# Kernel tuning notes

Measured on AMD Instinct MI355X. Metric: run time of the kernel, lower is better.

The kernel has to match this reference:

```python
import jax, jax.numpy as jnp
import numpy as np

EPS = 1e-05

def setup_inputs() -> dict:
    key = jax.random.key(0)
    k1, k2 = jax.random.split(key)
    B, C, H, W = 4, 512, 128, 128
    content_feat = jax.random.normal(k1, (B, C, H, W), dtype=jnp.float32)
    style_feat = jax.random.normal(k2, (B, C, H, W), dtype=jnp.float32)
    return {"content_feat": content_feat, "style_feat": style_feat}

def _cov(flat_centered, n):
    # flat_centered: [B, C, N] -> [B, C, C]
    C = flat_centered.shape[1]
    cov = jnp.einsum('bcn,bdn->bcd', flat_centered, flat_centered) / (n - 1)
    return cov + EPS * jnp.eye(C, dtype=flat_centered.dtype)

def reference(content_feat, style_feat):
    B, C, H, W = content_feat.shape
    N = H * W

    # --- whitening (content) ---
    cf = content_feat.reshape(B, C, -1)
    c_mean = jnp.mean(cf, axis=2, keepdims=True)
    c_cent = cf - c_mean
    c_cov = _cov(c_cent, N)
    u, s, vh = jnp.linalg.svd(c_cov)  # torch.svd's v == vh.T
    # u @ diag(s^-0.5) @ v^T @ c_cent
    whitened = jnp.einsum('bij,bj,bjk,bkn->bin', u, s ** -0.5, vh, c_cent)

    # --- coloring (style) ---
    sf = style_feat.reshape(B, C, -1)
    s_mean = jnp.mean(sf, axis=2, keepdims=True)
    s_cent = sf - s_mean
    s_cov = _cov(s_cent, N)
    su, ss, svh = jnp.linalg.svd(s_cov)
    colored = jnp.einsum('bij,bj,bjk,bkn->bin', su, jnp.sqrt(ss), svh, whitened)
    colored = colored + s_mean
    return colored.reshape(style_feat.shape)
```

## Files before the change

kernel.cpp:

```cpp
#include <hip/hip_runtime.h>


typedef unsigned short u16;
typedef __attribute__((ext_vector_type(8))) short bf16x8;
typedef __attribute__((ext_vector_type(4))) float f32x4;

__device__ __forceinline__ u16 f2bf(float f) {
  unsigned u = __float_as_uint(f);
  u += 0x7fffu + ((u >> 16) & 1u);
  return (u16)(u >> 16);
}

__device__ __forceinline__ void async_cp16(const u16* g, u16* l) {
  __builtin_amdgcn_global_load_lds((__attribute__((address_space(1))) void*)g,
                                   (__attribute__((address_space(3))) void*)l,
                                   16, 0, 0);
}

template<int BM, int BN, int FM, int FN>
__device__ __forceinline__ void gemm_nt(const u16* __restrict__ A, int lda,
                                        const u16* __restrict__ B, int ldb,
                                        int K, f32x4 (&acc)[FM][FN],
                                        u16* lA, u16* lB) {
  const int t = threadIdx.x;
  const int lane = t & 63;
  const int wid = t >> 6;
  const int wm = wid & 1, wn = wid >> 1;
  const int l16 = lane & 15, quad = lane >> 4;
  f32x4 zero = {0.f, 0.f, 0.f, 0.f};
#pragma unroll
  for (int im = 0; im < FM; ++im)
#pragma unroll
    for (int in = 0; in < FN; ++in) acc[im][in] = zero;

  constexpr int CA = (BM * 64) / (256 * 8);
  constexpr int CB = (BN * 64) / (256 * 8);

  for (int k0 = 0; k0 < K; k0 += 64) {
#pragma unroll
    for (int i = 0; i < CA; ++i) {
      int chunk = t + i * 256;
      async_cp16(A + (size_t)(chunk >> 3) * lda + k0 + (chunk & 7) * 8, lA + chunk * 8);
    }
#pragma unroll
    for (int i = 0; i < CB; ++i) {
      int chunk = t + i * 256;
      async_cp16(B + (size_t)(chunk >> 3) * ldb + k0 + (chunk & 7) * 8, lB + chunk * 8);
    }
    __syncthreads();
#pragma unroll
    for (int ks = 0; ks < 2; ++ks) {
      bf16x8 af[FM], bfr[FN];
#pragma unroll
      for (int im = 0; im < FM; ++im)
        af[im] = *(const bf16x8*)(lA + (wm * FM * 16 + im * 16 + l16) * 64 + ks * 32 + quad * 8);
#pragma unroll
      for (int in = 0; in < FN; ++in)
        bfr[in] = *(const bf16x8*)(lB + (wn * FN * 16 + in * 16 + l16) * 64 + ks * 32 + quad * 8);
#pragma unroll
      for (int im = 0; im < FM; ++im)
#pragma unroll
        for (int in = 0; in < FN; ++in)
          acc[im][in] = __builtin_amdgcn_mfma_f32_16x16x32_bf16(af[im], bfr[in], acc[im][in], 0, 0, 0);
    }
    __syncthreads();
  }
}

__global__ __launch_bounds__(256) void k_means_convert(
    const float* __restrict__ xc, const float* __restrict__ xs,
    u16* __restrict__ xcb, u16* __restrict__ xsb, float* __restrict__ mu) {
  int bx = blockIdx.x;
  int feat = bx >> 11;
  int row = bx & 2047;
  const float* src = (feat ? xs : xc) + (size_t)row * 16384;
  u16* dst = (feat ? xsb : xcb) + (size_t)row * 16384;
  int t = threadIdx.x;
  float s = 0.f;
#pragma unroll
  for (int i = 0; i < 16; ++i) {
    int idx = (t + i * 256) * 4;
    float4 v = *(const float4*)(src + idx);
    s += (v.x + v.y) + (v.z + v.w);
    ushort4 o;
    o.x = f2bf(v.x); o.y = f2bf(v.y); o.z = f2bf(v.z); o.w = f2bf(v.w);
    *(ushort4*)(dst + idx) = o;
  }
  __shared__ float red[256];
  red[t] = s;
  __syncthreads();
  for (int off = 128; off > 0; off >>= 1) {
    if (t < off) red[t] += red[t + off];
    __syncthreads();
  }
  if (t == 0) mu[bx] = red[0] * (1.f / 16384.f);
}

__global__ __launch_bounds__(256) void k_gram(
    const u16* __restrict__ xcb, const u16* __restrict__ xsb,
    const float* __restrict__ mu, float* __restrict__ cov) {
  __shared__ u16 lA[128 * 64], lB[128 * 64];
  const int tile = blockIdx.x, split = blockIdx.y, mat = blockIdx.z;
  const int tm = tile & 3, tn = tile >> 2;
  const u16* X = (mat >= 4 ? xsb : xcb) + (size_t)(mat & 3) * 512 * 16384;
  const u16* A = X + (size_t)tm * 128 * 16384 + split * 2048;
  const u16* B = X + (size_t)tn * 128 * 16384 + split * 2048;
  f32x4 acc[4][4];
  gemm_nt<128, 128, 4, 4>(A, 16384, B, 16384, 2048, acc, lA, lB);
  const int lane = threadIdx.x & 63, wid = threadIdx.x >> 6;
  const int wm = wid & 1, wn = wid >> 1, l16 = lane & 15, quad = lane >> 4;
  const float* muf = mu + (mat >> 2) * 2048 + (mat & 3) * 512;
  float* C = cov + (size_t)mat * 262144;
  const float scale = 1.f / 16383.f;
  const bool base = (split == 0);
#pragma unroll
  for (int im = 0; im < 4; ++im)
#pragma unroll
    for (int in = 0; in < 4; ++in)
#pragma unroll
      for (int i = 0; i < 4; ++i) {
        int gm = tm * 128 + wm * 64 + im * 16 + quad * 4 + i;
        int gn = tn * 128 + wn * 64 + in * 16 + l16;
        float v = acc[im][in][i] * scale;
        if (base) v += (gm == gn ? 1e-5f : 0.f) - (16384.f / 16383.f) * muf[gm] * muf[gn];
        atomicAdd(C + gm * 512 + gn, v);
      }
}

__global__ __launch_bounds__(256) void k_bound(const float* __restrict__ cov,
                                               float* __restrict__ lam) {
  const int mat = blockIdx.x, t = threadIdx.x;
  const float* A = cov + (size_t)mat * 262144;
  float mx = 0.f;
  for (int rr = 0; rr < 2; ++rr) {
    const float4* row = (const float4*)(A + (size_t)(t + rr * 256) * 512);
    float s = 0.f;
#pragma unroll 8
    for (int j = 0; j < 128; ++j) {
      float4 v = row[j];
      s += fabsf(v.x) + fabsf(v.y) + fabsf(v.z) + fabsf(v.w);
    }
    mx = fmaxf(mx, s);
  }
  __shared__ float red[256];
  red[t] = mx;
  __syncthreads();
  for (int off = 128; off > 0; off >>= 1) {
    if (t < off) red[t] = fmaxf(red[t], red[t + off]);
    __syncthreads();
  }
  if (t == 0) lam[mat] = red[0];
}

__global__ __launch_bounds__(256) void k_nsinit(
    const float* __restrict__ cov, const float* __restrict__ lam,
    const float* __restrict__ mu, float* __restrict__ Yfp, float* __restrict__ Zfp,
    u16* __restrict__ Ybf, u16* __restrict__ Zbf, float* __restrict__ bias) {
  int bx = blockIdx.x;
  if (bx >= 8192) {
    int i = (bx - 8192) * 256 + threadIdx.x;
    bias[i] = mu[2048 + i];
    return;
  }
  int mat = bx >> 10;
  int idx = (bx & 1023) * 256 + threadIdx.x;
  int i = idx >> 9, j = idx & 511;
  size_t g = (size_t)mat * 262144 + idx;
  float a = cov[g] / lam[mat];
  float z = (i == j) ? 1.f : 0.f;
  Yfp[g] = a; Zfp[g] = z;
  Ybf[g] = f2bf(a); Zbf[g] = f2bf(z);
}

__global__ __launch_bounds__(256) void k_ns1(const u16* __restrict__ Zbf,
                                             const u16* __restrict__ Ybf,
                                             u16* __restrict__ Dbf) {
  __shared__ u16 lA[64 * 64], lB[64 * 64];
  const int tile = blockIdx.x, mat = blockIdx.z;
  const int tm = tile & 7, tn = tile >> 3;
  const u16* A = Zbf + (size_t)mat * 262144 + tm * 64 * 512;
  const u16* B = Ybf + (size_t)mat * 262144 + tn * 64 * 512;
  f32x4 acc[2][2];
  gemm_nt<64, 64, 2, 2>(A, 512, B, 512, 512, acc, lA, lB);
  const int lane = threadIdx.x & 63, wid = threadIdx.x >> 6;
  const int wm = wid & 1, wn = wid >> 1, l16 = lane & 15, quad = lane >> 4;
  u16* D = Dbf + (size_t)mat * 262144;
#pragma unroll
  for (int im = 0; im < 2; ++im)
#pragma unroll
    for (int in = 0; in < 2; ++in)
#pragma unroll
      for (int i = 0; i < 4; ++i) {
        int gm = tm * 64 + wm * 32 + im * 16 + quad * 4 + i;
        int gn = tn * 64 + wn * 32 + in * 16 + l16;
        float d = 0.5f * ((gm == gn ? 1.f : 0.f) - acc[im][in][i]);
        D[gm * 512 + gn] = f2bf(d);
      }
}

__global__ __launch_bounds__(256) void k_ns2(
    const u16* __restrict__ Ybf, const u16* __restrict__ Zbf, const u16* __restrict__ Dbf,
    float* __restrict__ Yfp, float* __restrict__ Zfp,
    u16* __restrict__ Ybn, u16* __restrict__ Zbn) {
  __shared__ u16 lA[64 * 64], lB[64 * 64];
  const int tile = blockIdx.x, z = blockIdx.z;
  const int kind = z >> 3, mat = z & 7;
  const int tm = tile & 7, tn = tile >> 3;
  size_t mo = (size_t)mat * 262144;
  const u16* A; const u16* B; float* M; u16* O;
  if (kind == 0) { A = Ybf + mo; B = Dbf + mo; M = Yfp + mo; O = Ybn + mo; }
  else           { A = Dbf + mo; B = Zbf + mo; M = Zfp + mo; O = Zbn + mo; }
  f32x4 acc[2][2];
  gemm_nt<64, 64, 2, 2>(A + tm * 64 * 512, 512, B + tn * 64 * 512, 512, 512, acc, lA, lB);
  const int lane = threadIdx.x & 63, wid = threadIdx.x >> 6;
  const int wm = wid & 1, wn = wid >> 1, l16 = lane & 15, quad = lane >> 4;
#pragma unroll
  for (int im = 0; im < 2; ++im)
#pragma unroll
    for (int in = 0; in < 2; ++in)
#pragma unroll
      for (int i = 0; i < 4; ++i) {
        int gm = tm * 64 + wm * 32 + im * 16 + quad * 4 + i;
        int gn = tn * 64 + wn * 32 + in * 16 + l16;
        float v = acc[im][in][i] + M[gm * 512 + gn];
        M[gm * 512 + gn] = v;
        O[gm * 512 + gn] = f2bf(v);
      }
}

__global__ __launch_bounds__(256) void k_transpose(const u16* __restrict__ Xcb,
                                                   u16* __restrict__ Xct) {
  __shared__ u16 tb[64][72];
  const int t = threadIdx.x;
  const size_t base = (size_t)blockIdx.z * 512 * 16384;
  const int n0 = blockIdx.x * 64, c0 = blockIdx.y * 64;
#pragma unroll
  for (int i = 0; i < 2; ++i) {
    int chunk = t + i * 256;
    int r = chunk >> 3, cc = chunk & 7;
    uint4 v = *(const uint4*)(Xcb + base + (size_t)(c0 + r) * 16384 + n0 + cc * 8);
    const u16* e = (const u16*)&v;
#pragma unroll
    for (int j = 0; j < 8; ++j) tb[cc * 8 + j][r] = e[j];
  }
  __syncthreads();
  const size_t obase = (size_t)blockIdx.z * 16384 * 512;
#pragma unroll
  for (int i = 0; i < 2; ++i) {
    int chunk = t + i * 256;
    int r = chunk >> 3, cc = chunk & 7;
    u16 tmp[8];
#pragma unroll
    for (int j = 0; j < 8; ++j) tmp[j] = tb[r][cc * 8 + j];
    *(uint4*)(Xct + obase + (size_t)(n0 + r) * 512 + c0 + cc * 8) = *(const uint4*)tmp;
  }
}

__global__ __launch_bounds__(256) void k_compose(
    const u16* __restrict__ Ybf, const u16* __restrict__ Zbf,
    const float* __restrict__ lam, const float* __restrict__ mu,
    float* __restrict__ bias, u16* __restrict__ Tbf) {
  __shared__ u16 lA[128 * 64], lB[128 * 64];
  const int tile = blockIdx.x, b = blockIdx.z;
  const int tm = tile & 3, tn = tile >> 2;
  const u16* A = Ybf + (size_t)(4 + b) * 262144 + tm * 128 * 512;
  const u16* B = Zbf + (size_t)b * 262144 + tn * 128 * 512;
  f32x4 acc[4][4];
  gemm_nt<128, 128, 4, 4>(A, 512, B, 512, 512, acc, lA, lB);
  const int lane = threadIdx.x & 63, wid = threadIdx.x >> 6;
  const int wm = wid & 1, wn = wid >> 1, l16 = lane & 15, quad = lane >> 4;
  const float scale = sqrtf(lam[4 + b] / lam[b]);
  const float* muc = mu + b * 512;
  u16* T = Tbf + (size_t)b * 262144;
#pragma unroll
  for (int im = 0; im < 4; ++im)
#pragma unroll
    for (int i = 0; i < 4; ++i) {
      int gm = tm * 128 + wm * 64 + im * 16 + quad * 4 + i;
      float s = 0.f;
#pragma unroll
      for (int in = 0; in < 4; ++in) {
        int gn = tn * 128 + wn * 64 + in * 16 + l16;
        float tv = acc[im][in][i] * scale;
        T[gm * 512 + gn] = f2bf(tv);
        s += tv * muc[gn];
      }
      atomicAdd(&bias[b * 512 + gm], -s);
    }
}

__global__ __launch_bounds__(256) void k_apply(
    const u16* __restrict__ Tbf, const u16* __restrict__ Xct,
    const float* __restrict__ bias, float* __restrict__ out) {
  __shared__ u16 lA[128 * 64], lB[128 * 64];
  const int bx = blockIdx.x, b = blockIdx.z;
  const int tm = bx & 3, tn = bx >> 2;
  const u16* A = Tbf + (size_t)b * 262144 + tm * 128 * 512;
  const u16* B = Xct + (size_t)b * 16384 * 512 + (size_t)tn * 128 * 512;
  f32x4 acc[4][4];
  gemm_nt<128, 128, 4, 4>(A, 512, B, 512, 512, acc, lA, lB);
  const int lane = threadIdx.x & 63, wid = threadIdx.x >> 6;
  const int wm = wid & 1, wn = wid >> 1, l16 = lane & 15, quad = lane >> 4;
#pragma unroll
  for (int im = 0; im < 4; ++im)
#pragma unroll
    for (int in = 0; in < 4; ++in)
#pragma unroll
      for (int i = 0; i < 4; ++i) {
        int gm = tm * 128 + wm * 64 + im * 16 + quad * 4 + i;
        int gn = tn * 128 + wn * 64 + in * 16 + l16;
        out[((size_t)b * 512 + gm) * 16384 + gn] = acc[im][in][i] + bias[b * 512 + gm];
      }
}

extern "C" void kernel_launch(void* const* d_in, const int* in_sizes, int n_in,
                              void* d_out, int out_size, void* d_ws, size_t ws_size,
                              hipStream_t stream) {
  (void)in_sizes; (void)n_in; (void)out_size; (void)ws_size;
  const float* xc = (const float*)d_in[0];
  const float* xs = (const float*)d_in[1];
  float* out = (float*)d_out;
  char* w = (char*)d_ws;

  u16*   XA   = (u16*)(w);
  u16*   XB   = (u16*)(w + 67108864);
  float* cov  = (float*)(w + 134217728);
  float* Yfp  = (float*)(w + 142606336);
  float* Zfp  = (float*)(w + 150994944);
  u16*   Ybf0 = (u16*)(w + 159383552);
  u16*   Ybf1 = (u16*)(w + 163577856);
  u16*   Zbf0 = (u16*)(w + 167772160);
  u16*   Zbf1 = (u16*)(w + 171966464);
  u16*   Dbf  = (u16*)(w + 176160768);
  u16*   Tbf  = (u16*)(w + 180355072);
  float* mu   = (float*)(w + 182452224);
  float* lam  = (float*)(w + 182468608);
  float* bias = (float*)(w + 182468864);

  hipMemsetAsync(cov, 0, 8388608, stream);
  k_means_convert<<<4096, 256, 0, stream>>>(xc, xs, XA, XB, mu);
  k_gram<<<dim3(16, 8, 8), 256, 0, stream>>>(XA, XB, mu, cov);
  k_bound<<<8, 256, 0, stream>>>(cov, lam);
  k_nsinit<<<8200, 256, 0, stream>>>(cov, lam, mu, Yfp, Zfp, Ybf0, Zbf0, bias);
  k_transpose<<<dim3(256, 8, 4), 256, 0, stream>>>(XA, XB);

  u16 *Yc = Ybf0, *Yn = Ybf1, *Zc = Zbf0, *Zn = Zbf1;
  for (int it = 0; it < 8; ++it) {
    k_ns1<<<dim3(64, 1, 8), 256, 0, stream>>>(Zc, Yc, Dbf);
    k_ns2<<<dim3(64, 1, 16), 256, 0, stream>>>(Yc, Zc, Dbf, Yfp, Zfp, Yn, Zn);
    u16* t1 = Yc; Yc = Yn; Yn = t1;
    u16* t2 = Zc; Zc = Zn; Zn = t2;
  }

  k_compose<<<dim3(16, 1, 4), 256, 0, stream>>>(Yc, Zc, lam, mu, bias, Tbf);
  k_apply<<<dim3(512, 1, 4), 256, 0, stream>>>(Tbf, XB, bias, out);
}
```

Baseline: 923.7 us.

## Swizzle LDS layout, enlarge gram tiles with diagonal reuse, cut one NS iteration

The shared GEMM core now XOR-swizzles LDS rows to avoid bank conflicts, and its tile size, thread count and warp grid are templated. The Gram kernel moves to 256x256 tiles with 512 threads, and diagonal tiles reuse the A tile instead of staging B. The Newton-Schulz loop drops from 8 to 7 iterations, which removes work but may reduce the accuracy of the inverse square root. Larger tiles reduce the number of blocks and raise register pressure in the Gram kernel.

After: 871.7 us. -5.6%, faster.

```diff
diff --git a/kernel.cpp b/kernel.cpp
--- a/kernel.cpp
+++ b/kernel.cpp
@@ -17,35 +17,42 @@
                                    16, 0, 0);
 }
 
-template<int BM, int BN, int FM, int FN>
-__device__ __forceinline__ void gemm_nt(const u16* __restrict__ A, int lda,
-                                        const u16* __restrict__ B, int ldb,
-                                        int K, f32x4 (&acc)[FM][FN],
-                                        u16* lA, u16* lB) {
+template<int BM, int BN, int FM, int FN, int NT, int WM, int WN>
+__device__ __forceinline__ void gemm_core(const u16* __restrict__ A, int lda,
+                                          const u16* __restrict__ B, int ldb,
+                                          int K, f32x4 (&acc)[FM][FN],
+                                          u16* lA, u16* lB, bool stageB) {
   const int t = threadIdx.x;
   const int lane = t & 63;
   const int wid = t >> 6;
-  const int wm = wid & 1, wn = wid >> 1;
+  const int wm = wid % WM, wn = wid / WM;
   const int l16 = lane & 15, quad = lane >> 4;
+  const int sw = l16 & 7;
   f32x4 zero = {0.f, 0.f, 0.f, 0.f};
 #pragma unroll
   for (int im = 0; im < FM; ++im)
 #pragma unroll
     for (int in = 0; in < FN; ++in) acc[im][in] = zero;
 
-  constexpr int CA = (BM * 64) / (256 * 8);
-  constexpr int CB = (BN * 64) / (256 * 8);
+  constexpr int CA = (BM * 8) / NT;
+  constexpr int CB = (BN * 8) / NT;
 
   for (int k0 = 0; k0 < K; k0 += 64) {
 #pragma unroll
     for (int i = 0; i < CA; ++i) {
-      int chunk = t + i * 256;
-      async_cp16(A + (size_t)(chunk >> 3) * lda + k0 + (chunk & 7) * 8, lA + chunk * 8);
-    }
-#pragma unroll
-    for (int i = 0; i < CB; ++i) {
-      int chunk = t + i * 256;
-      async_cp16(B + (size_t)(chunk >> 3) * ldb + k0 + (chunk & 7) * 8, lB + chunk * 8);
+      int c = t + i * NT;
+      int row = c >> 3;
+      int src = (c & 7) ^ (row & 7);
+      async_cp16(A + (size_t)row * lda + k0 + src * 8, lA + c * 8);
+    }
+    if (stageB) {
+#pragma unroll
+      for (int i = 0; i < CB; ++i) {
+        int c = t + i * NT;
+        int row = c >> 3;
+        int src = (c & 7) ^ (row & 7);
+        async_cp16(B + (size_t)row * ldb + k0 + src * 8, lB + c * 8);
+      }
     }
     __syncthreads();
 #pragma unroll
@@ -53,10 +60,12 @@
       bf16x8 af[FM], bfr[FN];
 #pragma unroll
       for (int im = 0; im < FM; ++im)
-        af[im] = *(const bf16x8*)(lA + (wm * FM * 16 + im * 16 + l16) * 64 + ks * 32 + quad * 8);
+        af[im] = *(const bf16x8*)(lA + ((wm * FM + im) * 16 + l16) * 64 +
+                                  (((ks * 4 + quad) ^ sw) * 8));
 #pragma unroll
       for (int in = 0; in < FN; ++in)
-        bfr[in] = *(const bf16x8*)(lB + (wn * FN * 16 + in * 16 + l16) * 64 + ks * 32 + quad * 8);
+        bfr[in] = *(const bf16x8*)(lB + ((wn * FN + in) * 16 + l16) * 64 +
+                                   (((ks * 4 + quad) ^ sw) * 8));
 #pragma unroll
       for (int im = 0; im < FM; ++im)
 #pragma unroll
@@ -96,31 +105,33 @@
   if (t == 0) mu[bx] = red[0] * (1.f / 16384.f);
 }
 
-__global__ __launch_bounds__(256) void k_gram(
+__global__ __launch_bounds__(512, 2) void k_gram(
     const u16* __restrict__ xcb, const u16* __restrict__ xsb,
     const float* __restrict__ mu, float* __restrict__ cov) {
-  __shared__ u16 lA[128 * 64], lB[128 * 64];
+  __shared__ u16 lds[2 * 256 * 64];
   const int tile = blockIdx.x, split = blockIdx.y, mat = blockIdx.z;
-  const int tm = tile & 3, tn = tile >> 2;
+  const int tm = tile & 1, tn = tile >> 1;
   const u16* X = (mat >= 4 ? xsb : xcb) + (size_t)(mat & 3) * 512 * 16384;
-  const u16* A = X + (size_t)tm * 128 * 16384 + split * 2048;
-  const u16* B = X + (size_t)tn * 128 * 16384 + split * 2048;
-  f32x4 acc[4][4];
-  gemm_nt<128, 128, 4, 4>(A, 16384, B, 16384, 2048, acc, lA, lB);
-  const int lane = threadIdx.x & 63, wid = threadIdx.x >> 6;
-  const int wm = wid & 1, wn = wid >> 1, l16 = lane & 15, quad = lane >> 4;
+  const u16* A = X + (size_t)tm * 256 * 16384 + split * 2048;
+  const u16* B = X + (size_t)tn * 256 * 16384 + split * 2048;
+  u16* lA = lds;
+  u16* lB = (tm == tn) ? lds : lds + 256 * 64;
+  f32x4 acc[8][4];
+  gemm_core<256, 256, 8, 4, 512, 2, 4>(A, 16384, B, 16384, 2048, acc, lA, lB, tm != tn);
+  const int lane = threadIdx.x & 63, wid = threadIdx.x >> 6;
+  const int wm = wid % 2, wn = wid / 2, l16 = lane & 15, quad = lane >> 4;
   const float* muf = mu + (mat >> 2) * 2048 + (mat & 3) * 512;
   float* C = cov + (size_t)mat * 262144;
   const float scale = 1.f / 16383.f;
   const bool base = (split == 0);
 #pragma unroll
-  for (int im = 0; im < 4; ++im)
+  for (int im = 0; im < 8; ++im)
 #pragma unroll
     for (int in = 0; in < 4; ++in)
 #pragma unroll
       for (int i = 0; i < 4; ++i) {
-        int gm = tm * 128 + wm * 64 + im * 16 + quad * 4 + i;
-        int gn = tn * 128 + wn * 64 + in * 16 + l16;
+        int gm = tm * 256 + wm * 128 + im * 16 + quad * 4 + i;
+        int gn = tn * 256 + wn * 64 + in * 16 + l16;
         float v = acc[im][in][i] * scale;
         if (base) v += (gm == gn ? 1e-5f : 0.f) - (16384.f / 16383.f) * muf[gm] * muf[gn];
         atomicAdd(C + gm * 512 + gn, v);
@@ -175,15 +186,15 @@
 __global__ __launch_bounds__(256) void k_ns1(const u16* __restrict__ Zbf,
                                              const u16* __restrict__ Ybf,
                                              u16* __restrict__ Dbf) {
-  __shared__ u16 lA[64 * 64], lB[64 * 64];
+  __shared__ u16 lds[2 * 64 * 64];
   const int tile = blockIdx.x, mat = blockIdx.z;
   const int tm = tile & 7, tn = tile >> 3;
   const u16* A = Zbf + (size_t)mat * 262144 + tm * 64 * 512;
   const u16* B = Ybf + (size_t)mat * 262144 + tn * 64 * 512;
   f32x4 acc[2][2];
-  gemm_nt<64, 64, 2, 2>(A, 512, B, 512, 512, acc, lA, lB);
-  const int lane = threadIdx.x & 63, wid = threadIdx.x >> 6;
-  const int wm = wid & 1, wn = wid >> 1, l16 = lane & 15, quad = lane >> 4;
+  gemm_core<64, 64, 2, 2, 256, 2, 2>(A, 512, B, 512, 512, acc, lds, lds + 4096, true);
+  const int lane = threadIdx.x & 63, wid = threadIdx.x >> 6;
+  const int wm = wid % 2, wn = wid / 2, l16 = lane & 15, quad = lane >> 4;
   u16* D = Dbf + (size_t)mat * 262144;
 #pragma unroll
   for (int im = 0; im < 2; ++im)
@@ -202,7 +213,7 @@
     const u16* __restrict__ Ybf, const u16* __restrict__ Zbf, const u16* __restrict__ Dbf,
     float* __restrict__ Yfp, float* __restrict__ Zfp,
     u16* __restrict__ Ybn, u16* __restrict__ Zbn) {
-  __shared__ u16 lA[64 * 64], lB[64 * 64];
+  __shared__ u16 lds[2 * 64 * 64];
   const int tile = blockIdx.x, z = blockIdx.z;
   const int kind = z >> 3, mat = z & 7;
   const int tm = tile & 7, tn = tile >> 3;
@@ -211,9 +222,10 @@
   if (kind == 0) { A = Ybf + mo; B = Dbf + mo; M = Yfp + mo; O = Ybn + mo; }
   else           { A = Dbf + mo; B = Zbf + mo; M = Zfp + mo; O = Zbn + mo; }
   f32x4 acc[2][2];
-  gemm_nt<64, 64, 2, 2>(A + tm * 64 * 512, 512, B + tn * 64 * 512, 512, 512, acc, lA, lB);
-  const int lane = threadIdx.x & 63, wid = threadIdx.x >> 6;
-  const int wm = wid & 1, wn = wid >> 1, l16 = lane & 15, quad = lane >> 4;
+  gemm_core<64, 64, 2, 2, 256, 2, 2>(A + tm * 64 * 512, 512, B + tn * 64 * 512, 512, 512,
+                                     acc, lds, lds + 4096, true);
+  const int lane = threadIdx.x & 63, wid = threadIdx.x >> 6;
+  const int wm = wid % 2, wn = wid / 2, l16 = lane & 15, quad = lane >> 4;
 #pragma unroll
   for (int im = 0; im < 2; ++im)
 #pragma unroll
@@ -260,15 +272,15 @@
     const u16* __restrict__ Ybf, const u16* __restrict__ Zbf,
     const float* __restrict__ lam, const float* __restrict__ mu,
     float* __restrict__ bias, u16* __restrict__ Tbf) {
-  __shared__ u16 lA[128 * 64], lB[128 * 64];
+  __shared__ u16 lds[2 * 128 * 64];
   const int tile = blockIdx.x, b = blockIdx.z;
   const int tm = tile & 3, tn = tile >> 2;
   const u16* A = Ybf + (size_t)(4 + b) * 262144 + tm * 128 * 512;
   const u16* B = Zbf + (size_t)b * 262144 + tn * 128 * 512;
   f32x4 acc[4][4];
-  gemm_nt<128, 128, 4, 4>(A, 512, B, 512, 512, acc, lA, lB);
-  const int lane = threadIdx.x & 63, wid = threadIdx.x >> 6;
-  const int wm = wid & 1, wn = wid >> 1, l16 = lane & 15, quad = lane >> 4;
+  gemm_core<128, 128, 4, 4, 256, 2, 2>(A, 512, B, 512, 512, acc, lds, lds + 8192, true);
+  const int lane = threadIdx.x & 63, wid = threadIdx.x >> 6;
+  const int wm = wid % 2, wn = wid / 2, l16 = lane & 15, quad = lane >> 4;
   const float scale = sqrtf(lam[4 + b] / lam[b]);
   const float* muc = mu + b * 512;
   u16* T = Tbf + (size_t)b * 262144;
@@ -292,15 +304,15 @@
 __global__ __launch_bounds__(256) void k_apply(
     const u16* __restrict__ Tbf, const u16* __restrict__ Xct,
     const float* __restrict__ bias, float* __restrict__ out) {
-  __shared__ u16 lA[128 * 64], lB[128 * 64];
+  __shared__ u16 lds[2 * 128 * 64];
   const int bx = blockIdx.x, b = blockIdx.z;
   const int tm = bx & 3, tn = bx >> 2;
   const u16* A = Tbf + (size_t)b * 262144 + tm * 128 * 512;
   const u16* B = Xct + (size_t)b * 16384 * 512 + (size_t)tn * 128 * 512;
   f32x4 acc[4][4];
-  gemm_nt<128, 128, 4, 4>(A, 512, B, 512, 512, acc, lA, lB);
-  const int lane = threadIdx.x & 63, wid = threadIdx.x >> 6;
-  const int wm = wid & 1, wn = wid >> 1, l16 = lane & 15, quad = lane >> 4;
+  gemm_core<128, 128, 4, 4, 256, 2, 2>(A, 512, B, 512, 512, acc, lds, lds + 8192, true);
+  const int lane = threadIdx.x & 63, wid = threadIdx.x >> 6;
+  const int wm = wid % 2, wn = wid / 2, l16 = lane & 15, quad = lane >> 4;
 #pragma unroll
   for (int im = 0; im < 4; ++im)
 #pragma unroll
@@ -339,13 +351,13 @@
 
   hipMemsetAsync(cov, 0, 8388608, stream);
   k_means_convert<<<4096, 256, 0, stream>>>(xc, xs, XA, XB, mu);
-  k_gram<<<dim3(16, 8, 8), 256, 0, stream>>>(XA, XB, mu, cov);
+  k_gram<<<dim3(4, 8, 8), 512, 0, stream>>>(XA, XB, mu, cov);
   k_bound<<<8, 256, 0, stream>>>(cov, lam);
   k_nsinit<<<8200, 256, 0, stream>>>(cov, lam, mu, Yfp, Zfp, Ybf0, Zbf0, bias);
   k_transpose<<<dim3(256, 8, 4), 256, 0, stream>>>(XA, XB);
 
   u16 *Yc = Ybf0, *Yn = Ybf1, *Zc = Zbf0, *Zn = Zbf1;
-  for (int it = 0; it < 8; ++it) {
+  for (int it = 0; it < 7; ++it) {
     k_ns1<<<dim3(64, 1, 8), 256, 0, stream>>>(Zc, Yc, Dbf);
     k_ns2<<<dim3(64, 1, 16), 256, 0, stream>>>(Yc, Zc, Dbf, Yfp, Zfp, Yn, Zn);
     u16* t1 = Yc; Yc = Yn; Yn = t1;
```
